# Kernel tuning notes

Measured on AMD Instinct MI355X. Metric: run time of the kernel, lower is better.

## Reference

```python
import jax, jax.numpy as jnp
import numpy as np

T, H = 2048, 1024
NH, NKV, HD = 8, 2, 128
E, TOPK, NG, TKG = 16, 4, 4, 2
F, FS = 1024, 1024
EPS = 1e-6
ROUTED_SCALE = 2.0
THETA = 10000.0


def _rmsnorm(x, w):
    return x * jax.lax.rsqrt(jnp.mean(x * x, axis=-1, keepdims=True) + EPS) * w


def setup_inputs() -> dict:
    key = jax.random.key(0)
    ks = jax.random.split(key, 12)
    s = 0.02
    return {
        "hidden_states": jax.random.normal(ks[0], (T, H), jnp.float32),
        "residual": jax.random.normal(ks[1], (T, H), jnp.float32),
        "position_ids": jnp.arange(T, dtype=jnp.int32),
        "ln1_w": jnp.ones((H,), jnp.float32),
        "qkv_w": s * jax.random.normal(ks[2], (H, (NH + 2 * NKV) * HD), jnp.float32),
        "qnorm_w": jnp.ones((HD,), jnp.float32),
        "knorm_w": jnp.ones((HD,), jnp.float32),
        "dense_w": s * jax.random.normal(ks[3], (NH * HD, H), jnp.float32),
        "ln2_w": jnp.ones((H,), jnp.float32),
        "gate_w": s * jax.random.normal(ks[4], (H, E), jnp.float32),
        "expert_bias": 0.1 * jax.random.normal(ks[5], (E,), jnp.float32),
        "w13": s * jax.random.normal(ks[6], (E, H, 2 * F), jnp.float32),
        "w2": s * jax.random.normal(ks[7], (E, F, H), jnp.float32),
        "ws_gate_up": s * jax.random.normal(ks[8], (H, 2 * FS), jnp.float32),
        "ws_down": s * jax.random.normal(ks[9], (FS, H), jnp.float32),
    }


def block_forward(hidden_states, residual, position_ids, ln1_w, qkv_w, qnorm_w,
                  knorm_w, dense_w, ln2_w, gate_w, expert_bias, w13, w2,
                  ws_gate_up, ws_down):
    # fused add + RMSNorm (input_layernorm with residual)
    resid = hidden_states + residual
    h = _rmsnorm(resid, ln1_w)

    # --- attention ---
    qkv = h @ qkv_w  # [T, (NH+2*NKV)*HD]
    q = qkv[:, : NH * HD].reshape(T, NH, HD)
    k = qkv[:, NH * HD : (NH + NKV) * HD].reshape(T, NKV, HD)
    v = qkv[:, (NH + NKV) * HD :].reshape(T, NKV, HD)
    q = _rmsnorm(q, qnorm_w)  # qk-norm per head_dim
    k = _rmsnorm(k, knorm_w)

    # neox-style RoPE over full head_dim
    inv_freq = 1.0 / (THETA ** (jnp.arange(0, HD, 2, dtype=jnp.float32) / HD))
    ang = position_ids.astype(jnp.float32)[:, None] * inv_freq[None, :]  # [T, HD/2]
    cos = jnp.cos(ang)[:, None, :]
    sin = jnp.sin(ang)[:, None, :]

    def rope(x):
        x1, x2 = x[..., : HD // 2], x[..., HD // 2 :]
        return jnp.concatenate([x1 * cos - x2 * sin, x2 * cos + x1 * sin], axis=-1)

    q, k = rope(q), rope(k)
    rep = NH // NKV
    kr = jnp.repeat(k, rep, axis=1)  # [T, NH, HD]
    vr = jnp.repeat(v, rep, axis=1)

    scores = jnp.einsum("qhd,khd->hqk", q, kr) * (HD ** -0.5)
    causal = jnp.tril(jnp.ones((T, T), bool))
    scores = jnp.where(causal[None], scores, jnp.finfo(scores.dtype).min)
    probs = jax.nn.softmax(scores, axis=-1)
    ctx = jnp.einsum("hqk,khd->qhd", probs, vr).reshape(T, NH * HD)
    attn_out = ctx @ dense_w

    # fused add + RMSNorm (post_attention_layernorm)
    resid2 = attn_out + resid
    h2 = _rmsnorm(resid2, ln2_w)

    # --- MoE router: sigmoid scoring + correction bias, grouped top-k ---
    logits = h2.astype(jnp.float32) @ gate_w  # router in fp32
    s_scores = jax.nn.sigmoid(logits)  # [T, E]
    sfc = s_scores + expert_bias[None, :]
    gview = sfc.reshape(T, NG, E // NG)
    gscores = jax.lax.top_k(gview, 2)[0].sum(-1)  # sum of top-2 per group
    gidx = jax.lax.top_k(gscores, TKG)[1]  # [T, TKG]
    gmask = jax.nn.one_hot(gidx, NG, dtype=sfc.dtype).sum(1)  # [T, NG]
    smask = jnp.repeat(gmask, E // NG, axis=1)  # [T, E]
    masked = jnp.where(smask > 0, sfc, -jnp.inf)
    topk_idx = jax.lax.top_k(masked, TOPK)[1]  # [T, TOPK]
    topk_w = jnp.take_along_axis(s_scores, topk_idx, axis=1)  # weights w/o bias
    topk_w = topk_w / (topk_w.sum(-1, keepdims=True) + 1e-20)  # renormalize
    combine = (jax.nn.one_hot(topk_idx, E, dtype=topk_w.dtype) * topk_w[..., None]).sum(1)  # [T, E]

    # routed experts (dense-over-experts reference for the grouped GEMM)
    gu = jnp.einsum("th,ehf->tef", h2, w13)  # [T, E, 2F]
    g, u = gu[..., :F], gu[..., F:]
    act = jax.nn.silu(g) * u
    y = jnp.einsum("tef,efh->teh", act, w2)
    routed = jnp.einsum("teh,te->th", y, combine) * ROUTED_SCALE

    # shared expert (SwiGLU MLP)
    su = h2 @ ws_gate_up
    shared = (jax.nn.silu(su[:, :FS]) * su[:, FS:]) @ ws_down

    mlp_out = routed + shared
    return mlp_out, resid2


def reference(hidden_states, residual, position_ids, ln1_w, qkv_w, qnorm_w,
              knorm_w, dense_w, ln2_w, gate_w, expert_bias, w13, w2,
              ws_gate_up, ws_down):
    return block_forward(hidden_states, residual, position_ids, ln1_w, qkv_w,
                         qnorm_w, knorm_w, dense_w, ln2_w, gate_w, expert_bias,
                         w13, w2, ws_gate_up, ws_down)
```

## Files before the change

### kernel.cpp

```cpp
#include <hip/hip_runtime.h>
#include <hip/hip_bf16.h>


#define T_TOK 2048
#define H_DIM 1024
#define NHEAD 8
#define NKVH 2
#define HDIM 128
#define QKV_DIM 1536
#define E_EXP 16
#define TOPKE 4
#define F_DIM 1024
#define FS_DIM 1024
#define NPAIR (T_TOK*TOPKE)
#define EPS_F 1e-6f

#define DEV __device__ __forceinline__

typedef __attribute__((ext_vector_type(4))) float f32x4;
typedef __attribute__((ext_vector_type(8))) short s16x8;

DEV float us2f(unsigned short u){ return __uint_as_float(((unsigned int)u)<<16); }
DEV unsigned short f2us(float f){
  __hip_bfloat16 b = __float2bfloat16(f);
  unsigned short u; __builtin_memcpy(&u,&b,2); return u;
}

DEV void gl2lds16(const void* g, void* l){
  __builtin_amdgcn_global_load_lds(
      (const __attribute__((address_space(1))) void*)g,
      (__attribute__((address_space(3))) void*)l, 16, 0, 0);
}

DEV float bred_sum(float v, float* sm){
  #pragma unroll
  for(int o=32;o>0;o>>=1) v += __shfl_down(v,o);
  int w = threadIdx.x>>6, l = threadIdx.x&63;
  __syncthreads();
  if(l==0) sm[w]=v;
  __syncthreads();
  return sm[0]+sm[1]+sm[2]+sm[3];
}

__global__ __launch_bounds__(256) void k_cvt_t(const float* __restrict__ in,
    unsigned short* __restrict__ out, int Kd, int Nd){
  const int z = blockIdx.z;
  const int kb = blockIdx.y*32, nb = blockIdx.x*32;
  __shared__ float Lt[32][33];
  const int tid = threadIdx.x;
  const int r = tid>>3, c4 = (tid&7)*4;
  const float* src = in + (long long)z*Kd*Nd + (long long)(kb+r)*Nd + nb + c4;
  float4 v = *(const float4*)src;
  Lt[r][c4+0]=v.x; Lt[r][c4+1]=v.y; Lt[r][c4+2]=v.z; Lt[r][c4+3]=v.w;
  __syncthreads();
  ushort4 o;
  o.x = f2us(Lt[c4+0][r]); o.y = f2us(Lt[c4+1][r]);
  o.z = f2us(Lt[c4+2][r]); o.w = f2us(Lt[c4+3][r]);
  *(ushort4*)(out + (long long)z*Nd*Kd + (long long)(nb+r)*Kd + kb + c4) = o;
}

template<bool GROUPED, bool GATHER>
__global__ __launch_bounds__(256) void gemm_mfma(
    const unsigned short* __restrict__ A, int lda,
    const unsigned short* __restrict__ Bt, int ldbt, long long bstride,
    unsigned short* __restrict__ C, int ldc,
    const int* __restrict__ rowidx, const int* __restrict__ grpoff,
    int Mdense, int K){
  const int z = blockIdx.z;
  const int rb = GROUPED ? grpoff[z] : 0;
  const int re = GROUPED ? grpoff[z+1] : Mdense;
  const int m0 = rb + blockIdx.y*128;
  if(m0 >= re) return;
  const int n0 = blockIdx.x*128;
  const unsigned short* Bz = Bt + (long long)z*bstride;

  __shared__ unsigned short As[128][32];
  __shared__ unsigned short Bs[128][32];

  const int tid = threadIdx.x;
  const int s0 = tid, s1 = tid+256;
  int gr0 = m0 + (s0>>2), gr1 = m0 + (s1>>2);
  if(GROUPED){ gr0 = min(gr0, re-1); gr1 = min(gr1, re-1); }
  if(GATHER){ gr0 = rowidx[gr0]; gr1 = rowidx[gr1]; }
  const unsigned short* ag0 = A + (long long)gr0*lda + (s0&3)*8;
  const unsigned short* ag1 = A + (long long)gr1*lda + (s1&3)*8;
  const unsigned short* bg0 = Bz + (long long)(n0 + (s0>>2))*ldbt + (s0&3)*8;
  const unsigned short* bg1 = Bz + (long long)(n0 + (s1>>2))*ldbt + (s1&3)*8;
  char* asb = (char*)&As[0][0];
  char* bsb = (char*)&Bs[0][0];
  const int wb = (tid & 192)*16;

  const int w = tid>>6, lane = tid&63;
  const int wm = (w>>1)*64, wn = (w&1)*64;
  const int fr = lane&15, q8 = (lane>>4)*8;

  f32x4 zero = {0.f,0.f,0.f,0.f};
  f32x4 acc[4][4];
  #pragma unroll
  for(int mi=0;mi<4;mi++)
    #pragma unroll
    for(int ni=0;ni<4;ni++) acc[mi][ni]=zero;

  for(int k0=0;k0<K;k0+=32){
    __syncthreads();
    gl2lds16(ag0 + k0, asb + wb);
    gl2lds16(ag1 + k0, asb + 4096 + wb);
    gl2lds16(bg0 + k0, bsb + wb);
    gl2lds16(bg1 + k0, bsb + 4096 + wb);
    __syncthreads();
    s16x8 af[4], bf[4];
    #pragma unroll
    for(int mi=0;mi<4;mi++) af[mi] = *(const s16x8*)&As[wm+mi*16+fr][q8];
    #pragma unroll
    for(int ni=0;ni<4;ni++) bf[ni] = *(const s16x8*)&Bs[wn+ni*16+fr][q8];
    #pragma unroll
    for(int mi=0;mi<4;mi++)
      #pragma unroll
      for(int ni=0;ni<4;ni++)
        acc[mi][ni] = __builtin_amdgcn_mfma_f32_16x16x32_bf16(af[mi], bf[ni], acc[mi][ni], 0,0,0);
  }
  const int q4 = (lane>>4)*4;
  #pragma unroll
  for(int mi=0;mi<4;mi++)
    #pragma unroll
    for(int ni=0;ni<4;ni++){
      const int col = n0 + wn + ni*16 + fr;
      #pragma unroll
      for(int r=0;r<4;r++){
        const int row = m0 + wm + mi*16 + q4 + r;
        if(row < re) C[(long long)row*ldc + col] = f2us(acc[mi][ni][r]);
      }
    }
}

__global__ __launch_bounds__(256) void k_silu(const unsigned short* __restrict__ gu,
    unsigned short* __restrict__ act){
  const int r = blockIdx.x, c = threadIdx.x*4;
  const ushort4 g4 = *(const ushort4*)(gu + (long long)r*2048 + c);
  const ushort4 u4 = *(const ushort4*)(gu + (long long)r*2048 + 1024 + c);
  float g[4] = {us2f(g4.x),us2f(g4.y),us2f(g4.z),us2f(g4.w)};
  float u[4] = {us2f(u4.x),us2f(u4.y),us2f(u4.z),us2f(u4.w)};
  ushort4 o;
  o.x = f2us((g[0]/(1.f+__expf(-g[0])))*u[0]);
  o.y = f2us((g[1]/(1.f+__expf(-g[1])))*u[1]);
  o.z = f2us((g[2]/(1.f+__expf(-g[2])))*u[2]);
  o.w = f2us((g[3]/(1.f+__expf(-g[3])))*u[3]);
  *(ushort4*)(act + (long long)r*1024 + c) = o;
}

__global__ __launch_bounds__(256) void k_add_rmsnorm(const float* __restrict__ hs,
    const float* __restrict__ rs, const float* __restrict__ w,
    float* __restrict__ resid, float* __restrict__ h){
  int t = blockIdx.x, tid = threadIdx.x;
  __shared__ float sm[4];
  const long base = (long)t*H_DIM;
  float x[4]; float ss = 0.f;
  #pragma unroll
  for(int i=0;i<4;i++){
    int c = tid + i*256;
    float v = hs[base+c] + rs[base+c];
    x[i]=v; resid[base+c]=v; ss += v*v;
  }
  float tot = bred_sum(ss, sm);
  float rms = rsqrtf(tot/(float)H_DIM + EPS_F);
  #pragma unroll
  for(int i=0;i<4;i++){
    int c = tid + i*256;
    h[base+c] = x[i]*rms*w[c];
  }
}

template<int EPI_ADD>
__global__ __launch_bounds__(256) void gemm_f32(
    const float* __restrict__ A, int lda,
    const float* __restrict__ B, int ldb,
    float* __restrict__ C, int ldc,
    const float* __restrict__ D, int M, int K){
  const int m0 = blockIdx.y*128;
  const int n0 = blockIdx.x*64;
  __shared__ float As[16][132];
  __shared__ float Bs[16][65];
  float acc[8][4];
  #pragma unroll
  for(int i=0;i<8;i++)
    #pragma unroll
    for(int j=0;j<4;j++) acc[i][j]=0.f;
  const int tid = threadIdx.x;
  const int tx = tid & 15, ty = tid >> 4;
  const int ar = tid >> 1, ac = (tid & 1)*8;
  const int brr = tid >> 4, bc = (tid & 15)*4;
  const float* Aptr = A + (long long)(m0+ar)*lda;
  for(int k0=0;k0<K;k0+=16){
    float4 a0 = *(const float4*)(Aptr + k0 + ac);
    float4 a1 = *(const float4*)(Aptr + k0 + ac + 4);
    float4 bv = *(const float4*)(B + (long long)(k0+brr)*ldb + n0 + bc);
    __syncthreads();
    As[ac+0][ar]=a0.x; As[ac+1][ar]=a0.y; As[ac+2][ar]=a0.z; As[ac+3][ar]=a0.w;
    As[ac+4][ar]=a1.x; As[ac+5][ar]=a1.y; As[ac+6][ar]=a1.z; As[ac+7][ar]=a1.w;
    Bs[brr][bc+0]=bv.x; Bs[brr][bc+1]=bv.y; Bs[brr][bc+2]=bv.z; Bs[brr][bc+3]=bv.w;
    __syncthreads();
    #pragma unroll
    for(int kk=0;kk<16;kk++){
      float a[8], b[4];
      #pragma unroll
      for(int i=0;i<8;i++) a[i]=As[kk][ty*8+i];
      #pragma unroll
      for(int j=0;j<4;j++) b[j]=Bs[kk][tx*4+j];
      #pragma unroll
      for(int i=0;i<8;i++)
        #pragma unroll
        for(int j=0;j<4;j++) acc[i][j] = fmaf(a[i], b[j], acc[i][j]);
    }
  }
  #pragma unroll
  for(int i=0;i<8;i++){
    int r = m0 + ty*8 + i;
    float* crow = C + (long long)r*ldc + n0 + tx*4;
    float4 v = make_float4(acc[i][0],acc[i][1],acc[i][2],acc[i][3]);
    if(EPI_ADD){
      const float4 d = *(const float4*)(D + (long long)r*ldc + n0 + tx*4);
      v.x+=d.x; v.y+=d.y; v.z+=d.z; v.w+=d.w;
    }
    *(float4*)crow = v;
  }
}

__global__ __launch_bounds__(64) void k_qkv_post(const float* __restrict__ qkv,
    const float* __restrict__ qw, const float* __restrict__ kw,
    const int* __restrict__ pos,
    float* __restrict__ qb, float* __restrict__ kb, float* __restrict__ vb){
  int slot = blockIdx.x, t = blockIdx.y, lane = threadIdx.x;
  const float* x = qkv + (long long)t*QKV_DIM + slot*HDIM;
  float x0 = x[lane], x1 = x[lane+64];
  if(slot < 10){
    float ss = x0*x0 + x1*x1;
    #pragma unroll
    for(int o=32;o>0;o>>=1) ss += __shfl_xor(ss,o);
    float rms = rsqrtf(ss/(float)HDIM + EPS_F);
    const float* w = (slot<8)? qw : kw;
    float n0 = x0*rms*w[lane];
    float n1 = x1*rms*w[lane+64];
    float p = (float)pos[t];
    float invf = __expf(-((float)lane/64.f)*9.210340371976184f);
    float ang = p*invf;
    float s = sinf(ang), c = cosf(ang);
    float o0 = n0*c - n1*s;
    float o1 = n1*c + n0*s;
    float* dst = (slot<8)? (qb + ((long long)slot*T_TOK + t)*HDIM)
                         : (kb + ((long long)(slot-8)*T_TOK + t)*HDIM);
    dst[lane]=o0; dst[lane+64]=o1;
  } else {
    float* dst = vb + ((long long)(slot-10)*T_TOK + t)*HDIM;
    dst[lane]=x0; dst[lane+64]=x1;
  }
}

#define FBQ 32
#define FBK 128
__global__ __launch_bounds__(256,2) void k_flash(const float* __restrict__ qb,
    const float* __restrict__ kb, const float* __restrict__ vb,
    float* __restrict__ ctx){
  const int h = blockIdx.x;
  const int by = blockIdx.y;
  const int qt = (by < 32) ? (63 - by) : (by - 32);
  const int kv = h >> 2;
  const int q0 = qt * FBQ;
  const int tid = threadIdx.x;
  const int lane = tid & 63;
  const int w = tid >> 6;
  const int tx = tid & 31;
  const int ty = tid >> 5;
  const int fsw = tx & 7;

  __shared__ float4 smem4[4096];
  char*  smem = (char*)smem4;
  float* Ksf  = (float*)smem;
  float* Psf  = (float*)(smem + 49152);

  const float scale = 0.08838834764831845f;
  const float* kbase = kb + (long long)kv*T_TOK*HDIM;
  const float* vbase = vb + (long long)kv*T_TOK*HDIM;
  const float* qrow0 = qb + ((long long)h*T_TOK + q0 + ty*4)*HDIM;

  float m_[4], l_[4], O[4][4];
  #pragma unroll
  for(int qi=0;qi<4;qi++){
    m_[qi] = -1e30f; l_[qi] = 0.f;
    #pragma unroll
    for(int j=0;j<4;j++) O[qi][j] = 0.f;
  }

  const int nkt = (qt >> 2) + 1;

  for(int kt=0; kt<nkt; kt++){
    const int k0 = kt * FBK;
    __syncthreads();
    {
      const float* kcur = kbase + (long long)k0*HDIM;
      #pragma unroll
      for(int i=0;i<16;i++){
        const int rbase = (w<<5) + (i<<1);
        const int f = (i>>1) & 7;
        const float* src = kcur + (long long)(rbase + (lane>>5))*HDIM
                                + (((lane&31)^f)<<2);
        gl2lds16(src, smem + rbase*512);
      }
    }
    __syncthreads();

    float s[4][4];
    #pragma unroll
    for(int qi=0;qi<4;qi++)
      #pragma unroll
      for(int ki=0;ki<4;ki++) s[qi][ki] = 0.f;

    #pragma unroll 2
    for(int dc=0; dc<32; dc++){
      float4 qv[4];
      #pragma unroll
      for(int qi=0;qi<4;qi++) qv[qi] = *(const float4*)(qrow0 + qi*HDIM + dc*4);
      float4 kf[4];
      #pragma unroll
      for(int ki=0;ki<4;ki++)
        kf[ki] = *(const float4*)&Ksf[(size_t)(4*tx+ki)*128 + ((dc ^ fsw)<<2)];
      #pragma unroll
      for(int qi=0;qi<4;qi++)
        #pragma unroll
        for(int ki=0;ki<4;ki++){
          s[qi][ki] = fmaf(qv[qi].x, kf[ki].x, s[qi][ki]);
          s[qi][ki] = fmaf(qv[qi].y, kf[ki].y, s[qi][ki]);
          s[qi][ki] = fmaf(qv[qi].z, kf[ki].z, s[qi][ki]);
          s[qi][ki] = fmaf(qv[qi].w, kf[ki].w, s[qi][ki]);
        }
    }

    const bool last = (kt == nkt-1);
    float rm[4];
    #pragma unroll
    for(int qi=0;qi<4;qi++){
      #pragma unroll
      for(int ki=0;ki<4;ki++){
        float v = s[qi][ki]*scale;
        if(last && (k0 + 4*tx + ki > q0 + ty*4 + qi)) v = -1e30f;
        s[qi][ki] = v;
      }
      rm[qi] = fmaxf(fmaxf(s[qi][0],s[qi][1]), fmaxf(s[qi][2],s[qi][3]));
    }
    #pragma unroll
    for(int o=1;o<32;o<<=1){
      #pragma unroll
      for(int qi=0;qi<4;qi++) rm[qi] = fmaxf(rm[qi], __shfl_xor(rm[qi], o));
    }
    float a_[4], rs[4];
    #pragma unroll
    for(int qi=0;qi<4;qi++){
      float mn = fmaxf(m_[qi], rm[qi]);
      a_[qi] = __expf(m_[qi] - mn);
      m_[qi] = mn;
      float r = 0.f;
      #pragma unroll
      for(int ki=0;ki<4;ki++){ s[qi][ki] = __expf(s[qi][ki] - mn); r += s[qi][ki]; }
      rs[qi] = r;
    }
    #pragma unroll
    for(int o=1;o<32;o<<=1){
      #pragma unroll
      for(int qi=0;qi<4;qi++) rs[qi] += __shfl_xor(rs[qi], o);
    }
    #pragma unroll
    for(int qi=0;qi<4;qi++){
      l_[qi] = l_[qi]*a_[qi] + rs[qi];
      #pragma unroll
      for(int j=0;j<4;j++) O[qi][j] *= a_[qi];
    }

    __syncthreads();
    #pragma unroll
    for(int ki=0;ki<4;ki++){
      float4 pv;
      pv.x = s[0][ki]; pv.y = s[1][ki]; pv.z = s[2][ki]; pv.w = s[3][ki];
      *(float4*)&Psf[(size_t)(4*tx+ki)*32 + ((ty ^ fsw)<<2)] = pv;
    }
    __syncthreads();

    const float* vcur = vbase + (long long)k0*HDIM + tx*4;
    #pragma unroll 4
    for(int k=0;k<FBK;k++){
      float4 p4 = *(const float4*)&Psf[(size_t)k*32 + ((ty ^ ((k>>2)&7))<<2)];
      float4 vv = *(const float4*)(vcur + (size_t)k*HDIM);
      O[0][0]=fmaf(p4.x,vv.x,O[0][0]); O[0][1]=fmaf(p4.x,vv.y,O[0][1]);
      O[0][2]=fmaf(p4.x,vv.z,O[0][2]); O[0][3]=fmaf(p4.x,vv.w,O[0][3]);
      O[1][0]=fmaf(p4.y,vv.x,O[1][0]); O[1][1]=fmaf(p4.y,vv.y,O[1][1]);
      O[1][2]=fmaf(p4.y,vv.z,O[1][2]); O[1][3]=fmaf(p4.y,vv.w,O[1][3]);
      O[2][0]=fmaf(p4.z,vv.x,O[2][0]); O[2][1]=fmaf(p4.z,vv.y,O[2][1]);
      O[2][2]=fmaf(p4.z,vv.z,O[2][2]); O[2][3]=fmaf(p4.z,vv.w,O[2][3]);
      O[3][0]=fmaf(p4.w,vv.x,O[3][0]); O[3][1]=fmaf(p4.w,vv.y,O[3][1]);
      O[3][2]=fmaf(p4.w,vv.z,O[3][2]); O[3][3]=fmaf(p4.w,vv.w,O[3][3]);
    }
  }

  #pragma unroll
  for(int qi=0;qi<4;qi++){
    float inv = 1.f/l_[qi];
    float4 o4 = make_float4(O[qi][0]*inv, O[qi][1]*inv, O[qi][2]*inv, O[qi][3]*inv);
    *(float4*)(ctx + (long long)(q0 + ty*4 + qi)*(NHEAD*HDIM) + h*HDIM + tx*4) = o4;
  }
}

__global__ __launch_bounds__(256) void k_rms2(const float* __restrict__ r2,
    const float* __restrict__ w, float* __restrict__ h2f,
    unsigned short* __restrict__ h2b){
  int t = blockIdx.x, tid = threadIdx.x;
  __shared__ float sm[4];
  const long base = (long)t*H_DIM;
  float x[4]; float ss=0.f;
  #pragma unroll
  for(int i=0;i<4;i++){
    int c = tid+i*256;
    float v = r2[base+c];
    x[i]=v; ss += v*v;
  }
  float tot = bred_sum(ss, sm);
  float rms = rsqrtf(tot/(float)H_DIM + EPS_F);
  #pragma unroll
  for(int i=0;i<4;i++){
    int c = tid+i*256;
    float v = x[i]*rms*w[c];
    h2f[base+c] = v;
    h2b[base+c] = f2us(v);
  }
}

__global__ __launch_bounds__(256) void k_router(const float* __restrict__ h2,
    const float* __restrict__ gw, const float* __restrict__ eb,
    int* __restrict__ topk_idx, float* __restrict__ topk_w, int* __restrict__ counts){
  int t = blockIdx.x, tid = threadIdx.x;
  int e = tid & 15, seg = tid >> 4;
  const float* hrow = h2 + (long long)t*H_DIM;
  float part = 0.f;
  #pragma unroll 4
  for(int i=0;i<64;i++){
    int hh = seg*64 + i;
    part += hrow[hh]*gw[hh*E_EXP + e];
  }
  __shared__ float pm[16][17];
  __shared__ float sS[16], sfc[16];
  pm[seg][e] = part;
  __syncthreads();
  if(tid < 16){
    float l = 0.f;
    #pragma unroll
    for(int s=0;s<16;s++) l += pm[s][tid];
    float sg = 1.f/(1.f+expf(-l));
    sS[tid]=sg; sfc[tid]=sg+eb[tid];
  }
  __syncthreads();
  if(tid==0){
    float gs[4];
    #pragma unroll
    for(int g=0; g<4; g++){
      float m1=-1e30f, m2=-1e30f;
      for(int j=0;j<4;j++){
        float v=sfc[g*4+j];
        if(v>m1){ m2=m1; m1=v; } else if(v>m2){ m2=v; }
      }
      gs[g]=m1+m2;
    }
    int g1=0; for(int g=1;g<4;g++) if(gs[g]>gs[g1]) g1=g;
    int g2=-1; for(int g=0;g<4;g++){ if(g==g1) continue; if(g2<0||gs[g]>gs[g2]) g2=g; }
    bool taken[16];
    #pragma unroll
    for(int i=0;i<16;i++) taken[i]=false;
    int idx[4];
    for(int j=0;j<4;j++){
      int best=-1; float bv=-1e30f;
      for(int i=0;i<16;i++){
        int g=i>>2;
        if(g!=g1 && g!=g2) continue;
        if(taken[i]) continue;
        if(best<0 || sfc[i]>bv){ best=i; bv=sfc[i]; }
      }
      taken[best]=true; idx[j]=best;
    }
    float w[4]; float s=0.f;
    #pragma unroll
    for(int j=0;j<4;j++){ w[j]=sS[idx[j]]; s+=w[j]; }
    s += 1e-20f;
    #pragma unroll
    for(int j=0;j<4;j++){
      topk_idx[t*4+j]=idx[j];
      topk_w[t*4+j]=w[j]/s;
      atomicAdd(&counts[idx[j]],1);
    }
  }
}

__global__ void k_zero(int* __restrict__ counts){ if(threadIdx.x<16) counts[threadIdx.x]=0; }

__global__ void k_scan(const int* __restrict__ counts, int* __restrict__ offs, int* __restrict__ cursor){
  if(threadIdx.x==0){
    int s=0;
    for(int e2=0;e2<16;e2++){ offs[e2]=s; cursor[e2]=s; s+=counts[e2]; }
    offs[16]=s;
  }
}

__global__ __launch_bounds__(256) void k_scatter(const int* __restrict__ topk_idx,
    int* __restrict__ cursor, int* __restrict__ pair_tok, int* __restrict__ tok2pair){
  int i = blockIdx.x*256 + threadIdx.x;
  int e = topk_idx[i];
  int pos = atomicAdd(&cursor[e],1);
  pair_tok[pos] = i>>2;
  tok2pair[i] = pos;
}

__global__ __launch_bounds__(256) void k_combine(const unsigned short* __restrict__ y,
    const unsigned short* __restrict__ sout, const int* __restrict__ tok2pair,
    const float* __restrict__ topk_w, float* __restrict__ out0){
  int t = blockIdx.x, tid = threadIdx.x;
  int p[4]; float w[4];
  #pragma unroll
  for(int j=0;j<4;j++){ p[j]=tok2pair[t*4+j]; w[j]=topk_w[t*4+j]*2.0f; }
  const long base = (long)t*H_DIM;
  #pragma unroll
  for(int i=0;i<4;i++){
    int c = tid + i*256;
    float v = us2f(sout[base+c]);
    #pragma unroll
    for(int j=0;j<4;j++) v += w[j]*us2f(y[(long long)p[j]*H_DIM + c]);
    out0[base+c] = v;
  }
}

extern "C" void kernel_launch(void* const* d_in, const int* in_sizes, int n_in,
                              void* d_out, int out_size, void* d_ws, size_t ws_size,
                              hipStream_t stream) {
  const float* hs   = (const float*)d_in[0];
  const float* rsd  = (const float*)d_in[1];
  const int*   pos  = (const int*)d_in[2];
  const float* ln1  = (const float*)d_in[3];
  const float* qkvw = (const float*)d_in[4];
  const float* qnw  = (const float*)d_in[5];
  const float* knw  = (const float*)d_in[6];
  const float* dw   = (const float*)d_in[7];
  const float* ln2  = (const float*)d_in[8];
  const float* gw   = (const float*)d_in[9];
  const float* eb   = (const float*)d_in[10];
  const float* w13  = (const float*)d_in[11];
  const float* w2   = (const float*)d_in[12];
  const float* wsgu = (const float*)d_in[13];
  const float* wsd  = (const float*)d_in[14];
  float* out0 = (float*)d_out;
  float* out1 = out0 + (size_t)T_TOK*H_DIM;

  char* W = (char*)d_ws;
  float* resid = (float*)(W + 0);
  float* h     = (float*)(W + 8388608);
  float* ctx   = h;
  float* qkv   = (float*)(W + 16777216);
  float* qb    = (float*)(W + 29360128);
  float* h2f   = (float*)(W + 37748736);
  float* kb    = (float*)(W + 46137344);
  float* vb    = (float*)(W + 48234496);
  unsigned short* gu    = (unsigned short*)(W + 8388608);
  unsigned short* ybuf  = (unsigned short*)(W + 8388608);
  unsigned short* sgu   = (unsigned short*)(W + 16777216);
  unsigned short* sact  = (unsigned short*)(W + 0);
  unsigned short* sout  = (unsigned short*)(W + 46137344);
  unsigned short* h2b   = (unsigned short*)(W + 50331648);
  unsigned short* act   = (unsigned short*)(W + 54525952);
  unsigned short* w13t  = (unsigned short*)(W + 71303168);
  unsigned short* w2t   = (unsigned short*)(W + 138412032);
  unsigned short* wsgut = (unsigned short*)(W + 171966464);
  unsigned short* wsdt  = (unsigned short*)(W + 176160768);
  float* topkw = (float*)(W + 178257920);
  int* topki   = (int*)(W + 178290688);
  int* ptok    = (int*)(W + 178323456);
  int* t2p     = (int*)(W + 178356224);
  int* cnt     = (int*)(W + 178388992);
  int* offs    = (int*)(W + 178389056);
  int* cur     = (int*)(W + 178389184);

  k_cvt_t<<<dim3(64,32,16), 256, 0, stream>>>(w13,  w13t,  1024, 2048);
  k_cvt_t<<<dim3(32,32,16), 256, 0, stream>>>(w2,   w2t,   1024, 1024);
  k_cvt_t<<<dim3(64,32,1),  256, 0, stream>>>(wsgu, wsgut, 1024, 2048);
  k_cvt_t<<<dim3(32,32,1),  256, 0, stream>>>(wsd,  wsdt,  1024, 1024);
  k_add_rmsnorm<<<T_TOK, 256, 0, stream>>>(hs, rsd, ln1, resid, h);
  gemm_f32<0><<<dim3(QKV_DIM/64, T_TOK/128), 256, 0, stream>>>(
      h, H_DIM, qkvw, QKV_DIM, qkv, QKV_DIM, nullptr, T_TOK, H_DIM);
  k_qkv_post<<<dim3(12, T_TOK), 64, 0, stream>>>(qkv, qnw, knw, pos, qb, kb, vb);
  k_flash<<<dim3(NHEAD, 64), 256, 0, stream>>>(qb, kb, vb, ctx);
  gemm_f32<1><<<dim3(H_DIM/64, T_TOK/128), 256, 0, stream>>>(
      ctx, NHEAD*HDIM, dw, H_DIM, out1, H_DIM, resid, T_TOK, NHEAD*HDIM);
  k_rms2<<<T_TOK, 256, 0, stream>>>(out1, ln2, h2f, h2b);
  k_zero<<<1, 64, 0, stream>>>(cnt);
  k_router<<<T_TOK, 256, 0, stream>>>(h2f, gw, eb, topki, topkw, cnt);
  k_scan<<<1, 64, 0, stream>>>(cnt, offs, cur);
  k_scatter<<<NPAIR/256, 256, 0, stream>>>(topki, cur, ptok, t2p);
  gemm_mfma<false,false><<<dim3(16,16,1), 256, 0, stream>>>(
      h2b, 1024, wsgut, 1024, 0, sgu, 2048, nullptr, nullptr, T_TOK, 1024);
  k_silu<<<T_TOK, 256, 0, stream>>>(sgu, sact);
  gemm_mfma<false,false><<<dim3(8,16,1), 256, 0, stream>>>(
      sact, 1024, wsdt, 1024, 0, sout, 1024, nullptr, nullptr, T_TOK, 1024);
  gemm_mfma<true,true><<<dim3(16,64,16), 256, 0, stream>>>(
      h2b, 1024, w13t, 1024, (long long)2048*1024, gu, 2048, ptok, offs, 0, 1024);
  k_silu<<<NPAIR, 256, 0, stream>>>(gu, act);
  gemm_mfma<true,false><<<dim3(8,64,16), 256, 0, stream>>>(
      act, 1024, w2t, 1024, (long long)1024*1024, ybuf, 1024, nullptr, offs, 0, 1024);
  k_combine<<<T_TOK, 256, 0, stream>>>(ybuf, sout, t2p, topkw, out0);
}
```

Measured before the change: 1.120 ms.

## Split heavy causal query tiles across two blocks with a merge kernel

Result: faster. 1.088 ms (-2.9%).

```diff
diff --git a/kernel.cpp b/kernel.cpp
--- a/kernel.cpp
+++ b/kernel.cpp
@@ -259,10 +259,24 @@
 #define FBK 128
 __global__ __launch_bounds__(256,2) void k_flash(const float* __restrict__ qb,
     const float* __restrict__ kb, const float* __restrict__ vb,
-    float* __restrict__ ctx){
+    float* __restrict__ ctx, float* __restrict__ Opart, float* __restrict__ Mpart){
   const int h = blockIdx.x;
   const int by = blockIdx.y;
-  const int qt = (by < 32) ? (63 - by) : (by - 32);
+  int qt, c0, c1, nktf, pc;
+  bool heavy;
+  if(by < 64){
+    heavy = true;
+    qt = 63 - (by>>1);
+    nktf = (qt>>2) + 1;
+    const int h1 = nktf>>1;
+    pc = by & 1;
+    if(pc){ c0 = 0; c1 = h1; } else { c0 = h1; c1 = nktf; }
+  } else {
+    heavy = false;
+    qt = 95 - by;
+    nktf = (qt>>2) + 1;
+    c0 = 0; c1 = nktf; pc = 0;
+  }
   const int kv = h >> 2;
   const int q0 = qt * FBQ;
   const int tid = threadIdx.x;
@@ -290,9 +304,7 @@
     for(int j=0;j<4;j++) O[qi][j] = 0.f;
   }
 
-  const int nkt = (qt >> 2) + 1;
-
-  for(int kt=0; kt<nkt; kt++){
+  for(int kt=c0; kt<c1; kt++){
     const int k0 = kt * FBK;
     __syncthreads();
     {
@@ -334,7 +346,7 @@
         }
     }
 
-    const bool last = (kt == nkt-1);
+    const bool last = (kt == nktf-1);
     float rm[4];
     #pragma unroll
     for(int qi=0;qi<4;qi++){
@@ -399,12 +411,45 @@
     }
   }
 
-  #pragma unroll
-  for(int qi=0;qi<4;qi++){
-    float inv = 1.f/l_[qi];
-    float4 o4 = make_float4(O[qi][0]*inv, O[qi][1]*inv, O[qi][2]*inv, O[qi][3]*inv);
-    *(float4*)(ctx + (long long)(q0 + ty*4 + qi)*(NHEAD*HDIM) + h*HDIM + tx*4) = o4;
-  }
+  if(heavy){
+    #pragma unroll
+    for(int qi=0;qi<4;qi++){
+      const int qr = q0 + ty*4 + qi - 1024;
+      float* dst = Opart + ((size_t)((h<<10) + qr)*2 + pc)*128 + tx*4;
+      *(float4*)dst = make_float4(O[qi][0],O[qi][1],O[qi][2],O[qi][3]);
+      if(tx==0){
+        float* mlp = Mpart + ((size_t)((h<<10) + qr)*2 + pc)*2;
+        mlp[0] = m_[qi]; mlp[1] = l_[qi];
+      }
+    }
+  } else {
+    #pragma unroll
+    for(int qi=0;qi<4;qi++){
+      float inv = 1.f/l_[qi];
+      float4 o4 = make_float4(O[qi][0]*inv, O[qi][1]*inv, O[qi][2]*inv, O[qi][3]*inv);
+      *(float4*)(ctx + (long long)(q0 + ty*4 + qi)*(NHEAD*HDIM) + h*HDIM + tx*4) = o4;
+    }
+  }
+}
+
+__global__ __launch_bounds__(256) void k_fmerge(const float* __restrict__ Op,
+    const float* __restrict__ Ml, float* __restrict__ ctx){
+  const int wv = threadIdx.x>>6, lane = threadIdx.x&63;
+  const int r = blockIdx.x*4 + wv;
+  const int h = r>>10, qr = r&1023;
+  const float* o0 = Op + ((size_t)r*2+0)*128 + lane*2;
+  const float* o1 = Op + ((size_t)r*2+1)*128 + lane*2;
+  const float m0 = Ml[((size_t)r*2+0)*2+0], l0 = Ml[((size_t)r*2+0)*2+1];
+  const float m1 = Ml[((size_t)r*2+1)*2+0], l1 = Ml[((size_t)r*2+1)*2+1];
+  const float mx = fmaxf(m0,m1);
+  const float a0 = __expf(m0-mx), a1 = __expf(m1-mx);
+  const float li = 1.f/(l0*a0 + l1*a1);
+  float2 v0 = *(const float2*)o0;
+  float2 v1 = *(const float2*)o1;
+  float2 o;
+  o.x = (v0.x*a0 + v1.x*a1)*li;
+  o.y = (v0.y*a0 + v1.y*a1)*li;
+  *(float2*)(ctx + (size_t)(1024+qr)*(NHEAD*HDIM) + h*HDIM + lane*2) = o;
 }
 
 __global__ __launch_bounds__(256) void k_rms2(const float* __restrict__ r2,
@@ -562,6 +607,8 @@
   float* h2f   = (float*)(W + 37748736);
   float* kb    = (float*)(W + 46137344);
   float* vb    = (float*)(W + 48234496);
+  float* Opart = (float*)(W + 16777216);
+  float* Mpart = (float*)(W + 25165824);
   unsigned short* gu    = (unsigned short*)(W + 8388608);
   unsigned short* ybuf  = (unsigned short*)(W + 8388608);
   unsigned short* sgu   = (unsigned short*)(W + 16777216);
@@ -589,7 +636,8 @@
   gemm_f32<0><<<dim3(QKV_DIM/64, T_TOK/128), 256, 0, stream>>>(
       h, H_DIM, qkvw, QKV_DIM, qkv, QKV_DIM, nullptr, T_TOK, H_DIM);
   k_qkv_post<<<dim3(12, T_TOK), 64, 0, stream>>>(qkv, qnw, knw, pos, qb, kb, vb);
-  k_flash<<<dim3(NHEAD, 64), 256, 0, stream>>>(qb, kb, vb, ctx);
+  k_flash<<<dim3(NHEAD, 96), 256, 0, stream>>>(qb, kb, vb, ctx, Opart, Mpart);
+  k_fmerge<<<2048, 256, 0, stream>>>(Opart, Mpart, ctx);
   gemm_f32<1><<<dim3(H_DIM/64, T_TOK/128), 256, 0, stream>>>(
       ctx, NHEAD*HDIM, dw, H_DIM, out1, H_DIM, resid, T_TOK, NHEAD*HDIM);
   k_rms2<<<T_TOK, 256, 0, stream>>>(out1, ln2, h2f, h2b);
```

## Split causal flash attention into balanced KV-tile work units with merge pass

Applied to the files above, without the earlier changes.

Result: faster. 1.060 ms (-5.4%).

```diff
diff --git a/kernel.cpp b/kernel.cpp
--- a/kernel.cpp
+++ b/kernel.cpp
@@ -31,6 +31,8 @@
       (const __attribute__((address_space(1))) void*)g,
       (__attribute__((address_space(3))) void*)l, 16, 0, 0);
 }
+
+DEV int crow(int qt){ int a=qt>>2, b=qt&3; return (a+1)*(2*a+b); }
 
 DEV float bred_sum(float v, float* sm){
   #pragma unroll
@@ -259,12 +261,10 @@
 #define FBK 128
 __global__ __launch_bounds__(256,2) void k_flash(const float* __restrict__ qb,
     const float* __restrict__ kb, const float* __restrict__ vb,
-    float* __restrict__ ctx){
-  const int h = blockIdx.x;
-  const int by = blockIdx.y;
-  const int qt = (by < 32) ? (63 - by) : (by - 32);
-  const int kv = h >> 2;
-  const int q0 = qt * FBQ;
+    float* __restrict__ ctx, float* __restrict__ Op1, float* __restrict__ Op2,
+    float* __restrict__ Ml){
+  const int b = blockIdx.x;
+  const int u0 = (17*b)>>1, u1 = (17*(b+1))>>1;
   const int tid = threadIdx.x;
   const int lane = tid & 63;
   const int w = tid >> 6;
@@ -278,133 +278,208 @@
   float* Psf  = (float*)(smem + 49152);
 
   const float scale = 0.08838834764831845f;
-  const float* kbase = kb + (long long)kv*T_TOK*HDIM;
-  const float* vbase = vb + (long long)kv*T_TOK*HDIM;
-  const float* qrow0 = qb + ((long long)h*T_TOK + q0 + ty*4)*HDIM;
-
-  float m_[4], l_[4], O[4][4];
-  #pragma unroll
-  for(int qi=0;qi<4;qi++){
-    m_[qi] = -1e30f; l_[qi] = 0.f;
-    #pragma unroll
-    for(int j=0;j<4;j++) O[qi][j] = 0.f;
-  }
-
-  const int nkt = (qt >> 2) + 1;
-
-  for(int kt=0; kt<nkt; kt++){
-    const int k0 = kt * FBK;
-    __syncthreads();
+
+  int h = u0/544;
+  int r = u0 - h*544;
+  int qt = 0;
+  while(qt < 63 && crow(qt+1) <= r) qt++;
+  int kt = r - crow(qt);
+
+  int u = u0;
+  while(u < u1){
+    const int nkt = (qt>>2) + 1;
+    const int q0 = qt * FBQ;
+    const int kv = h >> 2;
+    const float* kbase = kb + (long long)kv*T_TOK*HDIM;
+    const float* vbase = vb + (long long)kv*T_TOK*HDIM;
+    const float* qrow0 = qb + ((long long)h*T_TOK + q0 + ty*4)*HDIM;
+    const int segN = min(nkt - kt, u1 - u);
+    const int ktEnd = kt + segN;
+
+    float m_[4], l_[4], O[4][4];
+    #pragma unroll
+    for(int qi=0;qi<4;qi++){
+      m_[qi] = -1e30f; l_[qi] = 0.f;
+      #pragma unroll
+      for(int j=0;j<4;j++) O[qi][j] = 0.f;
+    }
+
+    for(; kt<ktEnd; kt++){
+      const int k0 = kt * FBK;
+      __syncthreads();
+      {
+        const float* kcur = kbase + (long long)k0*HDIM;
+        #pragma unroll
+        for(int i=0;i<16;i++){
+          const int rbase = (w<<5) + (i<<1);
+          const int f = (i>>1) & 7;
+          const float* src = kcur + (long long)(rbase + (lane>>5))*HDIM
+                                  + (((lane&31)^f)<<2);
+          gl2lds16(src, smem + rbase*512);
+        }
+      }
+      __syncthreads();
+
+      float s[4][4];
+      #pragma unroll
+      for(int qi=0;qi<4;qi++)
+        #pragma unroll
+        for(int ki=0;ki<4;ki++) s[qi][ki] = 0.f;
+
+      #pragma unroll 2
+      for(int dc=0; dc<32; dc++){
+        float4 qv[4];
+        #pragma unroll
+        for(int qi=0;qi<4;qi++) qv[qi] = *(const float4*)(qrow0 + qi*HDIM + dc*4);
+        float4 kf[4];
+        #pragma unroll
+        for(int ki=0;ki<4;ki++)
+          kf[ki] = *(const float4*)&Ksf[(size_t)(4*tx+ki)*128 + ((dc ^ fsw)<<2)];
+        #pragma unroll
+        for(int qi=0;qi<4;qi++)
+          #pragma unroll
+          for(int ki=0;ki<4;ki++){
+            s[qi][ki] = fmaf(qv[qi].x, kf[ki].x, s[qi][ki]);
+            s[qi][ki] = fmaf(qv[qi].y, kf[ki].y, s[qi][ki]);
+            s[qi][ki] = fmaf(qv[qi].z, kf[ki].z, s[qi][ki]);
+            s[qi][ki] = fmaf(qv[qi].w, kf[ki].w, s[qi][ki]);
+          }
+      }
+
+      const bool last = (kt == nkt-1);
+      float rm[4];
+      #pragma unroll
+      for(int qi=0;qi<4;qi++){
+        #pragma unroll
+        for(int ki=0;ki<4;ki++){
+          float v = s[qi][ki]*scale;
+          if(last && (k0 + 4*tx + ki > q0 + ty*4 + qi)) v = -1e30f;
+          s[qi][ki] = v;
+        }
+        rm[qi] = fmaxf(fmaxf(s[qi][0],s[qi][1]), fmaxf(s[qi][2],s[qi][3]));
+      }
+      #pragma unroll
+      for(int o=1;o<32;o<<=1){
+        #pragma unroll
+        for(int qi=0;qi<4;qi++) rm[qi] = fmaxf(rm[qi], __shfl_xor(rm[qi], o));
+      }
+      float a_[4], rs[4];
+      #pragma unroll
+      for(int qi=0;qi<4;qi++){
+        float mn = fmaxf(m_[qi], rm[qi]);
+        a_[qi] = __expf(m_[qi] - mn);
+        m_[qi] = mn;
+        float rr = 0.f;
+        #pragma unroll
+        for(int ki=0;ki<4;ki++){ s[qi][ki] = __expf(s[qi][ki] - mn); rr += s[qi][ki]; }
+        rs[qi] = rr;
+      }
+      #pragma unroll
+      for(int o=1;o<32;o<<=1){
+        #pragma unroll
+        for(int qi=0;qi<4;qi++) rs[qi] += __shfl_xor(rs[qi], o);
+      }
+      #pragma unroll
+      for(int qi=0;qi<4;qi++){
+        l_[qi] = l_[qi]*a_[qi] + rs[qi];
+        #pragma unroll
+        for(int j=0;j<4;j++) O[qi][j] *= a_[qi];
+      }
+
+      __syncthreads();
+      #pragma unroll
+      for(int ki=0;ki<4;ki++){
+        float4 pv;
+        pv.x = s[0][ki]; pv.y = s[1][ki]; pv.z = s[2][ki]; pv.w = s[3][ki];
+        *(float4*)&Psf[(size_t)(4*tx+ki)*32 + ((ty ^ fsw)<<2)] = pv;
+      }
+      __syncthreads();
+
+      const float* vcur = vbase + (long long)k0*HDIM + tx*4;
+      #pragma unroll 4
+      for(int k=0;k<FBK;k++){
+        float4 p4 = *(const float4*)&Psf[(size_t)k*32 + ((ty ^ ((k>>2)&7))<<2)];
+        float4 vv = *(const float4*)(vcur + (size_t)k*HDIM);
+        O[0][0]=fmaf(p4.x,vv.x,O[0][0]); O[0][1]=fmaf(p4.x,vv.y,O[0][1]);
+        O[0][2]=fmaf(p4.x,vv.z,O[0][2]); O[0][3]=fmaf(p4.x,vv.w,O[0][3]);
+        O[1][0]=fmaf(p4.y,vv.x,O[1][0]); O[1][1]=fmaf(p4.y,vv.y,O[1][1]);
+        O[1][2]=fmaf(p4.y,vv.z,O[1][2]); O[1][3]=fmaf(p4.y,vv.w,O[1][3]);
+        O[2][0]=fmaf(p4.z,vv.x,O[2][0]); O[2][1]=fmaf(p4.z,vv.y,O[2][1]);
+        O[2][2]=fmaf(p4.z,vv.z,O[2][2]); O[2][3]=fmaf(p4.z,vv.w,O[2][3]);
+        O[3][0]=fmaf(p4.w,vv.x,O[3][0]); O[3][1]=fmaf(p4.w,vv.y,O[3][1]);
+        O[3][2]=fmaf(p4.w,vv.z,O[3][2]); O[3][3]=fmaf(p4.w,vv.w,O[3][3]);
+      }
+    }
+
     {
-      const float* kcur = kbase + (long long)k0*HDIM;
-      #pragma unroll
-      for(int i=0;i<16;i++){
-        const int rbase = (w<<5) + (i<<1);
-        const int f = (i>>1) & 7;
-        const float* src = kcur + (long long)(rbase + (lane>>5))*HDIM
-                                + (((lane&31)^f)<<2);
-        gl2lds16(src, smem + rbase*512);
-      }
-    }
-    __syncthreads();
-
-    float s[4][4];
-    #pragma unroll
-    for(int qi=0;qi<4;qi++)
-      #pragma unroll
-      for(int ki=0;ki<4;ki++) s[qi][ki] = 0.f;
-
-    #pragma unroll 2
-    for(int dc=0; dc<32; dc++){
-      float4 qv[4];
-      #pragma unroll
-      for(int qi=0;qi<4;qi++) qv[qi] = *(const float4*)(qrow0 + qi*HDIM + dc*4);
-      float4 kf[4];
-      #pragma unroll
-      for(int ki=0;ki<4;ki++)
-        kf[ki] = *(const float4*)&Ksf[(size_t)(4*tx+ki)*128 + ((dc ^ fsw)<<2)];
-      #pragma unroll
-      for(int qi=0;qi<4;qi++)
-        #pragma unroll
-        for(int ki=0;ki<4;ki++){
-          s[qi][ki] = fmaf(qv[qi].x, kf[ki].x, s[qi][ki]);
-          s[qi][ki] = fmaf(qv[qi].y, kf[ki].y, s[qi][ki]);
-          s[qi][ki] = fmaf(qv[qi].z, kf[ki].z, s[qi][ki]);
-          s[qi][ki] = fmaf(qv[qi].w, kf[ki].w, s[qi][ki]);
+      const int R = (h<<6) + qt;
+      const int S = h*544 + crow(qt);
+      const int bS = (2*S+1)/17;
+      const int j = b - bS;
+      #pragma unroll
+      for(int qi=0;qi<4;qi++){
+        const int row = ty*4 + qi;
+        float4 o4 = make_float4(O[qi][0],O[qi][1],O[qi][2],O[qi][3]);
+        if(j==0){
+          *(float4*)(ctx + (long long)(q0+row)*(NHEAD*HDIM) + h*HDIM + tx*4) = o4;
+        } else if(j==1){
+          *(float4*)(Op1 + (long long)R*4096 + row*128 + tx*4) = o4;
+        } else {
+          *(float4*)(Op2 + (long long)R*4096 + row*128 + tx*4) = o4;
         }
-    }
-
-    const bool last = (kt == nkt-1);
-    float rm[4];
-    #pragma unroll
-    for(int qi=0;qi<4;qi++){
-      #pragma unroll
-      for(int ki=0;ki<4;ki++){
-        float v = s[qi][ki]*scale;
-        if(last && (k0 + 4*tx + ki > q0 + ty*4 + qi)) v = -1e30f;
-        s[qi][ki] = v;
-      }
-      rm[qi] = fmaxf(fmaxf(s[qi][0],s[qi][1]), fmaxf(s[qi][2],s[qi][3]));
-    }
-    #pragma unroll
-    for(int o=1;o<32;o<<=1){
-      #pragma unroll
-      for(int qi=0;qi<4;qi++) rm[qi] = fmaxf(rm[qi], __shfl_xor(rm[qi], o));
-    }
-    float a_[4], rs[4];
-    #pragma unroll
-    for(int qi=0;qi<4;qi++){
-      float mn = fmaxf(m_[qi], rm[qi]);
-      a_[qi] = __expf(m_[qi] - mn);
-      m_[qi] = mn;
-      float r = 0.f;
-      #pragma unroll
-      for(int ki=0;ki<4;ki++){ s[qi][ki] = __expf(s[qi][ki] - mn); r += s[qi][ki]; }
-      rs[qi] = r;
-    }
-    #pragma unroll
-    for(int o=1;o<32;o<<=1){
-      #pragma unroll
-      for(int qi=0;qi<4;qi++) rs[qi] += __shfl_xor(rs[qi], o);
-    }
-    #pragma unroll
-    for(int qi=0;qi<4;qi++){
-      l_[qi] = l_[qi]*a_[qi] + rs[qi];
-      #pragma unroll
-      for(int j=0;j<4;j++) O[qi][j] *= a_[qi];
-    }
-
-    __syncthreads();
-    #pragma unroll
-    for(int ki=0;ki<4;ki++){
-      float4 pv;
-      pv.x = s[0][ki]; pv.y = s[1][ki]; pv.z = s[2][ki]; pv.w = s[3][ki];
-      *(float4*)&Psf[(size_t)(4*tx+ki)*32 + ((ty ^ fsw)<<2)] = pv;
-    }
-    __syncthreads();
-
-    const float* vcur = vbase + (long long)k0*HDIM + tx*4;
-    #pragma unroll 4
-    for(int k=0;k<FBK;k++){
-      float4 p4 = *(const float4*)&Psf[(size_t)k*32 + ((ty ^ ((k>>2)&7))<<2)];
-      float4 vv = *(const float4*)(vcur + (size_t)k*HDIM);
-      O[0][0]=fmaf(p4.x,vv.x,O[0][0]); O[0][1]=fmaf(p4.x,vv.y,O[0][1]);
-      O[0][2]=fmaf(p4.x,vv.z,O[0][2]); O[0][3]=fmaf(p4.x,vv.w,O[0][3]);
-      O[1][0]=fmaf(p4.y,vv.x,O[1][0]); O[1][1]=fmaf(p4.y,vv.y,O[1][1]);
-      O[1][2]=fmaf(p4.y,vv.z,O[1][2]); O[1][3]=fmaf(p4.y,vv.w,O[1][3]);
-      O[2][0]=fmaf(p4.z,vv.x,O[2][0]); O[2][1]=fmaf(p4.z,vv.y,O[2][1]);
-      O[2][2]=fmaf(p4.z,vv.z,O[2][2]); O[2][3]=fmaf(p4.z,vv.w,O[2][3]);
-      O[3][0]=fmaf(p4.w,vv.x,O[3][0]); O[3][1]=fmaf(p4.w,vv.y,O[3][1]);
-      O[3][2]=fmaf(p4.w,vv.z,O[3][2]); O[3][3]=fmaf(p4.w,vv.w,O[3][3]);
-    }
-  }
-
-  #pragma unroll
-  for(int qi=0;qi<4;qi++){
-    float inv = 1.f/l_[qi];
-    float4 o4 = make_float4(O[qi][0]*inv, O[qi][1]*inv, O[qi][2]*inv, O[qi][3]*inv);
-    *(float4*)(ctx + (long long)(q0 + ty*4 + qi)*(NHEAD*HDIM) + h*HDIM + tx*4) = o4;
-  }
+        if(tx==0){
+          Ml[((R*3+j)<<6) + row*2 + 0] = m_[qi];
+          Ml[((R*3+j)<<6) + row*2 + 1] = l_[qi];
+        }
+      }
+    }
+
+    u += segN;
+    if(ktEnd == nkt){ kt = 0; qt++; if(qt == 64){ qt = 0; h++; } }
+    else kt = ktEnd;
+  }
+}
+
+__global__ __launch_bounds__(256) void k_fmerge(float* __restrict__ ctx,
+    const float* __restrict__ Op1, const float* __restrict__ Op2,
+    const float* __restrict__ Ml){
+  const int wv = threadIdx.x>>6, lane = threadIdx.x&63;
+  const int gr = blockIdx.x*4 + wv;
+  const int R = gr>>5, q = gr&31;
+  const int h = R>>6, qt = R&63;
+  const int nkt = (qt>>2)+1;
+  const int S = h*544 + crow(qt);
+  const int bS = (2*S+1)/17;
+  const int bE = (2*(S+nkt-1)+1)/17;
+  const int parts = bE - bS + 1;
+  float* dst = ctx + (long long)(qt*32+q)*(NHEAD*HDIM) + h*HDIM + lane*2;
+  float2 o0 = *(float2*)dst;
+  const float* mlb = Ml + ((R*3)<<6) + q*2;
+  const float m0 = mlb[0], l0 = mlb[1];
+  float ox, oy;
+  if(parts == 1){
+    float inv = 1.f/l0;
+    ox = o0.x*inv; oy = o0.y*inv;
+  } else {
+    const float m1 = mlb[64], l1 = mlb[65];
+    float2 o1 = *(const float2*)(Op1 + (long long)R*4096 + q*128 + lane*2);
+    if(parts == 2){
+      float mx = fmaxf(m0,m1);
+      float a0 = __expf(m0-mx), a1 = __expf(m1-mx);
+      float inv = 1.f/(l0*a0 + l1*a1);
+      ox = (o0.x*a0 + o1.x*a1)*inv;
+      oy = (o0.y*a0 + o1.y*a1)*inv;
+    } else {
+      const float m2 = mlb[128], l2 = mlb[129];
+      float2 o2 = *(const float2*)(Op2 + (long long)R*4096 + q*128 + lane*2);
+      float mx = fmaxf(fmaxf(m0,m1),m2);
+      float a0 = __expf(m0-mx), a1 = __expf(m1-mx), a2 = __expf(m2-mx);
+      float inv = 1.f/(l0*a0 + l1*a1 + l2*a2);
+      ox = (o0.x*a0 + o1.x*a1 + o2.x*a2)*inv;
+      oy = (o0.y*a0 + o1.y*a1 + o2.y*a2)*inv;
+    }
+  }
+  dst[0] = ox; dst[1] = oy;
 }
 
 __global__ __launch_bounds__(256) void k_rms2(const float* __restrict__ r2,
@@ -562,6 +637,9 @@
   float* h2f   = (float*)(W + 37748736);
   float* kb    = (float*)(W + 46137344);
   float* vb    = (float*)(W + 48234496);
+  float* Op1   = (float*)(W + 16777216);
+  float* Ml    = (float*)(W + 25165824);
+  float* Op2   = (float*)(W + 37748736);
   unsigned short* gu    = (unsigned short*)(W + 8388608);
   unsigned short* ybuf  = (unsigned short*)(W + 8388608);
   unsigned short* sgu   = (unsigned short*)(W + 16777216);
@@ -589,7 +667,8 @@
   gemm_f32<0><<<dim3(QKV_DIM/64, T_TOK/128), 256, 0, stream>>>(
       h, H_DIM, qkvw, QKV_DIM, qkv, QKV_DIM, nullptr, T_TOK, H_DIM);
   k_qkv_post<<<dim3(12, T_TOK), 64, 0, stream>>>(qkv, qnw, knw, pos, qb, kb, vb);
-  k_flash<<<dim3(NHEAD, 64), 256, 0, stream>>>(qb, kb, vb, ctx);
+  k_flash<<<512, 256, 0, stream>>>(qb, kb, vb, ctx, Op1, Op2, Ml);
+  k_fmerge<<<4096, 256, 0, stream>>>(ctx, Op1, Op2, Ml);
   gemm_f32<1><<<dim3(H_DIM/64, T_TOK/128), 256, 0, stream>>>(
       ctx, NHEAD*HDIM, dw, H_DIM, out1, H_DIM, resid, T_TOK, NHEAD*HDIM);
   k_rms2<<<T_TOK, 256, 0, stream>>>(out1, ln2, h2f, h2b);
```
